# Optimization experiments

Hardware: AMD Instinct MI355X
Metric: run time of the kernel (lower is better)

The kernel has to match this reference:

```python
import jax, jax.numpy as jnp
import numpy as np

NUM_CLASSES = 96
T = 27          # max label slots per sample (hardcoded `range(1, 27)` in source)
NEG = -1e9      # finite stand-in for -inf masking (sim values are in [-1, 1])


def setup_inputs() -> dict:
    key = jax.random.key(0)
    k1, k2, k3 = jax.random.split(key, 3)
    B, D = 256, 1024
    input_f = jax.random.normal(k1, (B, T, D), dtype=jnp.float32)
    # labels in [1, 95]; zero is the end-of-word terminator
    tgt = jax.random.randint(k2, (B, T), 1, NUM_CLASSES, dtype=jnp.int32)
    lens = jax.random.randint(k3, (B,), 5, T, dtype=jnp.int32)  # first zero at position lens >= 1
    tgt = jnp.where(jnp.arange(T)[None, :] >= lens[:, None], 0, tgt)
    return {"input_f": input_f, "target": tgt}


def reference(input_f, target):
    B, Tt, D = input_f.shape
    # first zero position in target[:, 1:] gives the ragged prefix length per sample
    fz = jnp.argmax(target[:, 1:] == 0, axis=1) + 1            # [B], in [1, T-1]
    valid = jnp.arange(Tt)[None, :] < fz[:, None]              # [B, T] prefix mask (t=0 always valid)
    m = valid.reshape(-1)                                      # [B*T]

    # L2-normalize all rows (padded rows are masked out of the loss below)
    f = input_f.reshape(-1, D)
    f = f / jnp.clip(jnp.linalg.norm(f, axis=1, keepdims=True), 1e-12)
    sim = f @ f.T                                              # [N, N], N = B*T

    lab = target.reshape(-1)
    same = lab[:, None] == lab[None, :]                        # label_encode @ label_encode.T == 1
    pair_valid = m[:, None] & m[None, :]

    eye = jnp.eye(m.shape[0], dtype=bool)
    # multi-positive cross entropy (QDTrack-style):
    # loss_i = log(1 + sum_{pos p, neg n} exp(sim_in - sim_ip))
    #        = softplus(logsumexp_n(sim_in) + logsumexp_p(-sim_ip))
    pos_mask = (pair_valid & same) | (~m[:, None] & eye)       # give invalid rows a dummy entry
    neg_mask = (pair_valid & ~same) | (~m[:, None] & eye)
    lse_pos = jax.nn.logsumexp(jnp.where(pos_mask, -sim, NEG), axis=1)
    lse_neg = jax.nn.logsumexp(jnp.where(neg_mask, sim, NEG), axis=1)
    row_loss = jax.nn.softplus(lse_pos + lse_neg)

    n_valid = jnp.sum(m.astype(sim.dtype))
    return jnp.sum(jnp.where(m, row_loss, 0.0)) / n_valid
```

## Files before the change

kernel.cpp:

```cpp
#include <hip/hip_runtime.h>
#include <hip/hip_bf16.h>
#include <stdint.h>

#define BATCH 256
#define TSLOT 27
#define NTOT  (BATCH * TSLOT)
#define DIM   1024
#define TS    192
#define NSMAX 36
#define NTRIMAX (NSMAX * (NSMAX + 1) / 2)
#define KST   16
#define BUFSZ 24576
#define NBUF  6

typedef __attribute__((ext_vector_type(4))) float f32x4;
typedef __attribute__((ext_vector_type(2))) long l64x2;

__global__ __launch_bounds__(256) void prep_norm_kernel(const float* __restrict__ in,
                                                        const int* __restrict__ tgt,
                                                        unsigned char* __restrict__ cfb,
                                                        int* __restrict__ clab,
                                                        int* __restrict__ meta,
                                                        float* __restrict__ accum,
                                                        int* __restrict__ counter) {
    __shared__ int shs[256];
    __shared__ int shf[256];
    const int b = threadIdx.x;
    {
        const int* t = tgt + b * TSLOT;
        int fz = TSLOT;
        #pragma unroll
        for (int i = TSLOT - 1; i >= 1; --i) fz = (t[i] == 0) ? i : fz;
        shf[b] = fz;
        shs[b] = fz;
    }
    __syncthreads();
    for (int d = 1; d < 256; d <<= 1) {
        int v = (b >= d) ? shs[b - d] : 0;
        __syncthreads();
        shs[b] += v;
        __syncthreads();
    }
    const int nv = shs[255];
    const int npad = ((nv + TS - 1) / TS) * TS;

    if (blockIdx.x == 0) {
        if (b < 2) accum[b] = 0.0f;
        if (b == 2) *counter = 0;
        if (b == 3) { meta[0] = nv; meta[1] = npad; }
        if (b < npad - nv) clab[nv + b] = -1;
    }

    const int wv   = blockIdx.x * 4 + (threadIdx.x >> 6);
    const int lane = threadIdx.x & 63;
    const int bb = wv / TSLOT, tt = wv - bb * TSLOT;
    const int fzb = shf[bb];
    if (tt >= fzb) return;
    const int dest = (shs[bb] - fzb) + tt;

    const float* src = in + (size_t)wv * DIM + lane * 16;
    float4 v0 = *(const float4*)(src);
    float4 v1 = *(const float4*)(src + 4);
    float4 v2 = *(const float4*)(src + 8);
    float4 v3 = *(const float4*)(src + 12);
    float ss = v0.x*v0.x + v0.y*v0.y + v0.z*v0.z + v0.w*v0.w
             + v1.x*v1.x + v1.y*v1.y + v1.z*v1.z + v1.w*v1.w
             + v2.x*v2.x + v2.y*v2.y + v2.z*v2.z + v2.w*v2.w
             + v3.x*v3.x + v3.y*v3.y + v3.z*v3.z + v3.w*v3.w;
    #pragma unroll
    for (int off = 1; off < 64; off <<= 1) ss += __shfl_xor(ss, off);
    const float sc = 1.0f / fmaxf(sqrtf(ss), 1e-12f);
    float f[16] = {v0.x,v0.y,v0.z,v0.w, v1.x,v1.y,v1.z,v1.w,
                   v2.x,v2.y,v2.z,v2.w, v3.x,v3.y,v3.z,v3.w};
    uint4 o;
    unsigned int* ow = (unsigned int*)&o;
    #pragma unroll
    for (int q = 0; q < 4; ++q) {
        unsigned int u = 0;
        u = __builtin_amdgcn_cvt_pk_fp8_f32(f[q*4+0] * sc, f[q*4+1] * sc, u, 0);
        u = __builtin_amdgcn_cvt_pk_fp8_f32(f[q*4+2] * sc, f[q*4+3] * sc, u, 1);
        ow[q] = u;
    }
    *(uint4*)(cfb + (size_t)dest * DIM + lane * 16) = o;
    if (lane == 0) clab[dest] = tgt[wv];
}

__global__ __launch_bounds__(512) void gemm_kernel(const unsigned char* __restrict__ fb,
                                                   const int* __restrict__ clab,
                                                   const int* __restrict__ meta,
                                                   float* __restrict__ Ppos,
                                                   float* __restrict__ Pneg) {
    __shared__ __align__(16) char lds[NBUF * BUFSZ];

    const int npad = meta[1];
    const int nstrips = npad / TS;
    const int nact = nstrips * (nstrips + 1) / 2;
    const int k = blockIdx.x >> 3, x = blockIdx.x & 7;
    const int q8 = nact >> 3, r8 = nact & 7;
    const int cnt = q8 + (x < r8 ? 1 : 0);
    if (k >= cnt) return;
    int t = x * q8 + (x < r8 ? x : r8) + k;
    int bi = 0;
    while (t >= nstrips - bi) { t -= nstrips - bi; ++bi; }
    const int bj = bi + t;
    const int row0 = bi * TS;
    const int col0 = bj * TS;
    const bool diag = (bi == bj);

    const int tid  = threadIdx.x;
    const int lane = tid & 63;
    const int w    = tid >> 6;
    const int wm   = w >> 2;
    const int wn   = w & 3;

    f32x4 acc[6][3] = {};
    const char* fbyte = (const char*)fb;

    auto stage = [&](int s) {
        char* buf = lds + (s % NBUF) * BUFSZ;
        const int k0b = s * 64;
        #pragma unroll
        for (int j = 0; j < 3; ++j) {
            const int c = w * 192 + j * 64 + lane;
            const int cc = (c >= 768) ? c - 768 : c;
            const int base = (c >= 768) ? col0 : row0;
            const int r = cc >> 2, ks = cc & 3;
            const char* g = fbyte + (size_t)(base + r) * DIM + k0b + ks * 16;
            __builtin_amdgcn_global_load_lds(
                (const __attribute__((address_space(1))) void*)g,
                (__attribute__((address_space(3))) void*)(buf + c * 16),
                16, 0, 0);
        }
    };

    const int rsel = lane & 15, tsl = lane >> 4;
    auto compute = [&](int s) {
        const char* bA = lds + (s % NBUF) * BUFSZ;
        const char* bB = bA + 12288;
        l64x2 av[6], bv[3];
        #pragma unroll
        for (int m = 0; m < 6; ++m) {
            const int r = wm * 96 + m * 16 + rsel;
            av[m] = *(const l64x2*)(bA + r * 64 + tsl * 16);
        }
        #pragma unroll
        for (int n = 0; n < 3; ++n) {
            const int r = wn * 48 + n * 16 + rsel;
            bv[n] = *(const l64x2*)(bB + r * 64 + tsl * 16);
        }
        #pragma unroll
        for (int kk = 0; kk < 2; ++kk)
            #pragma unroll
            for (int m = 0; m < 6; ++m)
                #pragma unroll
                for (int n = 0; n < 3; ++n)
                    acc[m][n] = __builtin_amdgcn_mfma_f32_16x16x32_fp8_fp8(
                        av[m][kk], bv[n][kk], acc[m][n], 0, 0, 0);
    };

    stage(0); stage(1); stage(2); stage(3); stage(4);
    #pragma unroll 1
    for (int s = 0; s < KST - 5; ++s) {
        asm volatile("s_waitcnt vmcnt(12)" ::: "memory");
        __builtin_amdgcn_s_barrier();
        asm volatile("" ::: "memory");
        stage(s + 5);
        compute(s);
    }
    asm volatile("s_waitcnt vmcnt(12)" ::: "memory");
    __builtin_amdgcn_s_barrier();
    asm volatile("" ::: "memory");
    compute(KST - 5);
    asm volatile("s_waitcnt vmcnt(9)" ::: "memory");
    __builtin_amdgcn_s_barrier();
    asm volatile("" ::: "memory");
    compute(KST - 4);
    asm volatile("s_waitcnt vmcnt(6)" ::: "memory");
    __builtin_amdgcn_s_barrier();
    asm volatile("" ::: "memory");
    compute(KST - 3);
    asm volatile("s_waitcnt vmcnt(3)" ::: "memory");
    __builtin_amdgcn_s_barrier();
    asm volatile("" ::: "memory");
    compute(KST - 2);
    asm volatile("s_waitcnt vmcnt(0)" ::: "memory");
    __builtin_amdgcn_s_barrier();
    asm volatile("" ::: "memory");
    compute(KST - 1);

    const int c = rsel, g = tsl;
    float cpos[3] = {0, 0, 0}, cneg[3] = {0, 0, 0};
    float* fl = (float*)lds;

    #pragma unroll
    for (int m = 0; m < 6; ++m) {
        #pragma unroll
        for (int rg = 0; rg < 4; ++rg) {
            const int gi = row0 + wm * 96 + m * 16 + g * 4 + rg;
            const int li = clab[gi];
            float rp = 0.0f, rn = 0.0f;
            #pragma unroll
            for (int n = 0; n < 3; ++n) {
                const int gj = col0 + wn * 48 + n * 16 + c;
                const int lj = clab[gj];
                const float s = acc[m][n][rg];
                if (li >= 0 && lj >= 0) {
                    if (li == lj) { float e = __expf(-s); rp += e; cpos[n] += e; }
                    else          { float e = __expf(s);  rn += e; cneg[n] += e; }
                }
            }
            #pragma unroll
            for (int off = 1; off <= 8; off <<= 1) {
                rp += __shfl_xor(rp, off);
                rn += __shfl_xor(rn, off);
            }
            if (c == 0) {
                int lr = m * 16 + g * 4 + rg;
                fl[w * 96 + lr]        = rp;
                fl[768 + w * 96 + lr]  = rn;
            }
        }
    }
    #pragma unroll
    for (int n = 0; n < 3; ++n) {
        float p = cpos[n], q = cneg[n];
        p += __shfl_xor(p, 16); p += __shfl_xor(p, 32);
        q += __shfl_xor(q, 16); q += __shfl_xor(q, 32);
        if (g == 0) {
            int lc = n * 16 + c;
            fl[1536 + w * 48 + lc] = p;
            fl[1920 + w * 48 + lc] = q;
        }
    }
    __syncthreads();
    if (tid < 192) {
        int sm = tid / 96, lr = tid % 96;
        float rp = 0.0f, rn = 0.0f;
        #pragma unroll
        for (int kk = 0; kk < 4; ++kk) {
            rp += fl[(sm * 4 + kk) * 96 + lr];
            rn += fl[768 + (sm * 4 + kk) * 96 + lr];
        }
        int gi = row0 + tid;
        Ppos[(size_t)bj * NTOT + gi] = rp;
        Pneg[(size_t)bj * NTOT + gi] = rn;
    } else if (tid < 384 && !diag) {
        int j = tid - 192, cn = j / 48, lc = j % 48;
        float p = fl[1536 + cn * 48 + lc] + fl[1536 + (4 + cn) * 48 + lc];
        float q = fl[1920 + cn * 48 + lc] + fl[1920 + (4 + cn) * 48 + lc];
        int gj = col0 + j;
        Ppos[(size_t)bi * NTOT + gj] = p;
        Pneg[(size_t)bi * NTOT + gj] = q;
    }
}

__global__ __launch_bounds__(256) void finalize_kernel(const int* __restrict__ clab,
                                                       const int* __restrict__ meta,
                                                       const float* __restrict__ Ppos,
                                                       const float* __restrict__ Pneg,
                                                       float* __restrict__ accum,
                                                       int* __restrict__ counter,
                                                       float* __restrict__ out) {
    int i = blockIdx.x * blockDim.x + threadIdx.x;
    const int npad = meta[1];
    const int nta = npad / TS;
    float s = 0.0f, cnt = 0.0f;
    if (i < npad && clab[i] >= 0) {
        float sp = 0.0f, sn = 0.0f;
        for (int t = 0; t < nta; ++t) {
            sp += Ppos[(size_t)t * NTOT + i];
            sn += Pneg[(size_t)t * NTOT + i];
        }
        s = log1pf(sp * sn);
        cnt = 1.0f;
    }
    #pragma unroll
    for (int off = 1; off < 64; off <<= 1) {
        s   += __shfl_xor(s, off);
        cnt += __shfl_xor(cnt, off);
    }
    __shared__ float sh[8];
    int lane = threadIdx.x & 63, w = threadIdx.x >> 6;
    if (lane == 0) { sh[w] = s; sh[4 + w] = cnt; }
    __syncthreads();
    if (threadIdx.x == 0) {
        atomicAdd(&accum[0], sh[0] + sh[1] + sh[2] + sh[3]);
        atomicAdd(&accum[1], sh[4] + sh[5] + sh[6] + sh[7]);
        __threadfence();
        int done = atomicAdd(counter, 1);
        if (done == (int)gridDim.x - 1) {
            __threadfence();
            out[0] = accum[0] / accum[1];
        }
    }
}

extern "C" void kernel_launch(void* const* d_in, const int* in_sizes, int n_in,
                              void* d_out, int out_size, void* d_ws, size_t ws_size,
                              hipStream_t stream) {
    (void)in_sizes; (void)n_in; (void)out_size; (void)ws_size;
    const float* input_f = (const float*)d_in[0];
    const int*   target  = (const int*)d_in[1];
    float* out = (float*)d_out;

    char* ws = (char*)d_ws;
    const size_t FB_BYTES = (size_t)NTOT * DIM;
    unsigned char* cfb = (unsigned char*)ws;
    char* p = ws + FB_BYTES;
    int*   clab  = (int*)p;            p += NTOT * 4;
    int*   meta  = (int*)p;            p += 256;
    float* accum = (float*)p;          p += 128;
    int*   counter = (int*)p;          p += 128;
    float* Ppos  = (float*)p;          p += (size_t)NSMAX * NTOT * 4;
    float* Pneg  = (float*)p;

    prep_norm_kernel<<<dim3(NTOT / 4), dim3(256), 0, stream>>>(input_f, target, cfb, clab, meta, accum, counter);
    gemm_kernel<<<dim3(NTRIMAX), dim3(512), 0, stream>>>(cfb, clab, meta, Ppos, Pneg);
    finalize_kernel<<<dim3((NTOT + 255) / 256), dim3(256), 0, stream>>>(clab, meta, Ppos, Pneg, accum, counter, out);
}
```

Measured before the change: 50.08 us.

## Fuse prep, GEMM and finalize into one cooperative persistent kernel

```diff
diff --git a/kernel.cpp b/kernel.cpp
--- a/kernel.cpp
+++ b/kernel.cpp
@@ -1,6 +1,9 @@
 #include <hip/hip_runtime.h>
 #include <hip/hip_bf16.h>
+#include <hip/hip_cooperative_groups.h>
 #include <stdint.h>
+
+namespace cg = cooperative_groups;
 
 #define BATCH 256
 #define TSLOT 27
@@ -8,289 +11,290 @@
 #define DIM   1024
 #define TS    192
 #define NSMAX 36
-#define NTRIMAX (NSMAX * (NSMAX + 1) / 2)
 #define KST   16
 #define BUFSZ 24576
 #define NBUF  6
+#define NBLK  256
 
 typedef __attribute__((ext_vector_type(4))) float f32x4;
 typedef __attribute__((ext_vector_type(2))) long l64x2;
 
-__global__ __launch_bounds__(256) void prep_norm_kernel(const float* __restrict__ in,
-                                                        const int* __restrict__ tgt,
-                                                        unsigned char* __restrict__ cfb,
-                                                        int* __restrict__ clab,
-                                                        int* __restrict__ meta,
-                                                        float* __restrict__ accum,
-                                                        int* __restrict__ counter) {
+__global__ __launch_bounds__(512, 1)
+void fused_kernel(const float* __restrict__ in,
+                  const int* __restrict__ tgt,
+                  unsigned char* __restrict__ cfb,
+                  int* __restrict__ clab,
+                  float* __restrict__ Ppos,
+                  float* __restrict__ Pneg,
+                  float* __restrict__ accum,
+                  int* __restrict__ counter,
+                  float* __restrict__ out) {
+    __shared__ __align__(16) char lds[NBUF * BUFSZ];
     __shared__ int shs[256];
     __shared__ int shf[256];
-    const int b = threadIdx.x;
-    {
-        const int* t = tgt + b * TSLOT;
+
+    const int tid  = threadIdx.x;
+    const int lane = tid & 63;
+    const int w    = tid >> 6;
+    cg::grid_group grid = cg::this_grid();
+
+    if (tid < 256) {
+        const int* t = tgt + tid * TSLOT;
         int fz = TSLOT;
         #pragma unroll
         for (int i = TSLOT - 1; i >= 1; --i) fz = (t[i] == 0) ? i : fz;
-        shf[b] = fz;
-        shs[b] = fz;
+        shf[tid] = fz;
+        shs[tid] = fz;
     }
     __syncthreads();
     for (int d = 1; d < 256; d <<= 1) {
-        int v = (b >= d) ? shs[b - d] : 0;
+        int v = 0;
+        if (tid < 256 && tid >= d) v = shs[tid - d];
         __syncthreads();
-        shs[b] += v;
+        if (tid < 256) shs[tid] += v;
         __syncthreads();
     }
     const int nv = shs[255];
     const int npad = ((nv + TS - 1) / TS) * TS;
+    const int nstrips = npad / TS;
 
     if (blockIdx.x == 0) {
-        if (b < 2) accum[b] = 0.0f;
-        if (b == 2) *counter = 0;
-        if (b == 3) { meta[0] = nv; meta[1] = npad; }
-        if (b < npad - nv) clab[nv + b] = -1;
-    }
-
-    const int wv   = blockIdx.x * 4 + (threadIdx.x >> 6);
-    const int lane = threadIdx.x & 63;
-    const int bb = wv / TSLOT, tt = wv - bb * TSLOT;
-    const int fzb = shf[bb];
-    if (tt >= fzb) return;
-    const int dest = (shs[bb] - fzb) + tt;
-
-    const float* src = in + (size_t)wv * DIM + lane * 16;
-    float4 v0 = *(const float4*)(src);
-    float4 v1 = *(const float4*)(src + 4);
-    float4 v2 = *(const float4*)(src + 8);
-    float4 v3 = *(const float4*)(src + 12);
-    float ss = v0.x*v0.x + v0.y*v0.y + v0.z*v0.z + v0.w*v0.w
-             + v1.x*v1.x + v1.y*v1.y + v1.z*v1.z + v1.w*v1.w
-             + v2.x*v2.x + v2.y*v2.y + v2.z*v2.z + v2.w*v2.w
-             + v3.x*v3.x + v3.y*v3.y + v3.z*v3.z + v3.w*v3.w;
-    #pragma unroll
-    for (int off = 1; off < 64; off <<= 1) ss += __shfl_xor(ss, off);
-    const float sc = 1.0f / fmaxf(sqrtf(ss), 1e-12f);
-    float f[16] = {v0.x,v0.y,v0.z,v0.w, v1.x,v1.y,v1.z,v1.w,
-                   v2.x,v2.y,v2.z,v2.w, v3.x,v3.y,v3.z,v3.w};
-    uint4 o;
-    unsigned int* ow = (unsigned int*)&o;
-    #pragma unroll
-    for (int q = 0; q < 4; ++q) {
-        unsigned int u = 0;
-        u = __builtin_amdgcn_cvt_pk_fp8_f32(f[q*4+0] * sc, f[q*4+1] * sc, u, 0);
-        u = __builtin_amdgcn_cvt_pk_fp8_f32(f[q*4+2] * sc, f[q*4+3] * sc, u, 1);
-        ow[q] = u;
-    }
-    *(uint4*)(cfb + (size_t)dest * DIM + lane * 16) = o;
-    if (lane == 0) clab[dest] = tgt[wv];
-}
-
-__global__ __launch_bounds__(512) void gemm_kernel(const unsigned char* __restrict__ fb,
-                                                   const int* __restrict__ clab,
-                                                   const int* __restrict__ meta,
-                                                   float* __restrict__ Ppos,
-                                                   float* __restrict__ Pneg) {
-    __shared__ __align__(16) char lds[NBUF * BUFSZ];
-
-    const int npad = meta[1];
-    const int nstrips = npad / TS;
-    const int nact = nstrips * (nstrips + 1) / 2;
-    const int k = blockIdx.x >> 3, x = blockIdx.x & 7;
-    const int q8 = nact >> 3, r8 = nact & 7;
-    const int cnt = q8 + (x < r8 ? 1 : 0);
-    if (k >= cnt) return;
-    int t = x * q8 + (x < r8 ? x : r8) + k;
-    int bi = 0;
-    while (t >= nstrips - bi) { t -= nstrips - bi; ++bi; }
-    const int bj = bi + t;
-    const int row0 = bi * TS;
-    const int col0 = bj * TS;
-    const bool diag = (bi == bj);
-
-    const int tid  = threadIdx.x;
-    const int lane = tid & 63;
-    const int w    = tid >> 6;
-    const int wm   = w >> 2;
-    const int wn   = w & 3;
-
-    f32x4 acc[6][3] = {};
-    const char* fbyte = (const char*)fb;
-
-    auto stage = [&](int s) {
-        char* buf = lds + (s % NBUF) * BUFSZ;
-        const int k0b = s * 64;
+        if (tid < 2) accum[tid] = 0.0f;
+        if (tid == 2) *counter = 0;
+        if (tid < npad - nv) clab[nv + tid] = -1;
+    }
+
+    for (int wv = blockIdx.x * 8 + w; wv < NTOT; wv += NBLK * 8) {
+        const int bb = wv / TSLOT, tt = wv - bb * TSLOT;
+        const int fzb = shf[bb];
+        if (tt >= fzb) continue;
+        const int dest = (shs[bb] - fzb) + tt;
+
+        const float* src = in + (size_t)wv * DIM + lane * 16;
+        float4 v0 = *(const float4*)(src);
+        float4 v1 = *(const float4*)(src + 4);
+        float4 v2 = *(const float4*)(src + 8);
+        float4 v3 = *(const float4*)(src + 12);
+        float ss = v0.x*v0.x + v0.y*v0.y + v0.z*v0.z + v0.w*v0.w
+                 + v1.x*v1.x + v1.y*v1.y + v1.z*v1.z + v1.w*v1.w
+                 + v2.x*v2.x + v2.y*v2.y + v2.z*v2.z + v2.w*v2.w
+                 + v3.x*v3.x + v3.y*v3.y + v3.z*v3.z + v3.w*v3.w;
         #pragma unroll
-        for (int j = 0; j < 3; ++j) {
-            const int c = w * 192 + j * 64 + lane;
-            const int cc = (c >= 768) ? c - 768 : c;
-            const int base = (c >= 768) ? col0 : row0;
-            const int r = cc >> 2, ks = cc & 3;
-            const char* g = fbyte + (size_t)(base + r) * DIM + k0b + ks * 16;
-            __builtin_amdgcn_global_load_lds(
-                (const __attribute__((address_space(1))) void*)g,
-                (__attribute__((address_space(3))) void*)(buf + c * 16),
-                16, 0, 0);
-        }
-    };
-
-    const int rsel = lane & 15, tsl = lane >> 4;
-    auto compute = [&](int s) {
-        const char* bA = lds + (s % NBUF) * BUFSZ;
-        const char* bB = bA + 12288;
-        l64x2 av[6], bv[3];
+        for (int off = 1; off < 64; off <<= 1) ss += __shfl_xor(ss, off);
+        const float sc = 1.0f / fmaxf(sqrtf(ss), 1e-12f);
+        float f[16] = {v0.x,v0.y,v0.z,v0.w, v1.x,v1.y,v1.z,v1.w,
+                       v2.x,v2.y,v2.z,v2.w, v3.x,v3.y,v3.z,v3.w};
+        uint4 o;
+        unsigned int* ow = (unsigned int*)&o;
         #pragma unroll
-        for (int m = 0; m < 6; ++m) {
-            const int r = wm * 96 + m * 16 + rsel;
-            av[m] = *(const l64x2*)(bA + r * 64 + tsl * 16);
-        }
-        #pragma unroll
-        for (int n = 0; n < 3; ++n) {
-            const int r = wn * 48 + n * 16 + rsel;
-            bv[n] = *(const l64x2*)(bB + r * 64 + tsl * 16);
-        }
-        #pragma unroll
-        for (int kk = 0; kk < 2; ++kk)
+        for (int q = 0; q < 4; ++q) {
+            unsigned int u = 0;
+            u = __builtin_amdgcn_cvt_pk_fp8_f32(f[q*4+0] * sc, f[q*4+1] * sc, u, 0);
+            u = __builtin_amdgcn_cvt_pk_fp8_f32(f[q*4+2] * sc, f[q*4+3] * sc, u, 1);
+            ow[q] = u;
+        }
+        *(uint4*)(cfb + (size_t)dest * DIM + lane * 16) = o;
+        if (lane == 0) clab[dest] = tgt[wv];
+    }
+
+    grid.sync();
+
+    {
+        const int nact = nstrips * (nstrips + 1) / 2;
+        const int x = blockIdx.x & 7, kb0 = blockIdx.x >> 3;
+        const int q8 = nact >> 3, r8 = nact & 7;
+        const int cnt = q8 + (x < r8 ? 1 : 0);
+        const int wm = w >> 2;
+        const int wn = w & 3;
+        const int rsel = lane & 15, tsl = lane >> 4;
+        const char* fbyte = (const char*)cfb;
+
+        for (int kt = kb0; kt < cnt; kt += 32) {
+            int t = x * q8 + (x < r8 ? x : r8) + kt;
+            int bi = 0;
+            while (t >= nstrips - bi) { t -= nstrips - bi; ++bi; }
+            const int bj = bi + t;
+            const int row0 = bi * TS;
+            const int col0 = bj * TS;
+            const bool diag = (bi == bj);
+
+            f32x4 acc[6][3] = {};
+
+            auto stage = [&](int s) {
+                char* buf = lds + (s % NBUF) * BUFSZ;
+                const int k0b = s * 64;
+                #pragma unroll
+                for (int j = 0; j < 3; ++j) {
+                    const int c = w * 192 + j * 64 + lane;
+                    const int cc = (c >= 768) ? c - 768 : c;
+                    const int base = (c >= 768) ? col0 : row0;
+                    const int r = cc >> 2, ks = cc & 3;
+                    const char* g = fbyte + (size_t)(base + r) * DIM + k0b + ks * 16;
+                    __builtin_amdgcn_global_load_lds(
+                        (const __attribute__((address_space(1))) void*)g,
+                        (__attribute__((address_space(3))) void*)(buf + c * 16),
+                        16, 0, 0);
+                }
+            };
+            auto compute = [&](int s) {
+                const char* bA = lds + (s % NBUF) * BUFSZ;
+                const char* bB = bA + 12288;
+                l64x2 av[6], bv[3];
+                #pragma unroll
+                for (int m = 0; m < 6; ++m) {
+                    const int r = wm * 96 + m * 16 + rsel;
+                    av[m] = *(const l64x2*)(bA + r * 64 + tsl * 16);
+                }
+                #pragma unroll
+                for (int n = 0; n < 3; ++n) {
+                    const int r = wn * 48 + n * 16 + rsel;
+                    bv[n] = *(const l64x2*)(bB + r * 64 + tsl * 16);
+                }
+                #pragma unroll
+                for (int kk = 0; kk < 2; ++kk)
+                    #pragma unroll
+                    for (int m = 0; m < 6; ++m)
+                        #pragma unroll
+                        for (int n = 0; n < 3; ++n)
+                            acc[m][n] = __builtin_amdgcn_mfma_f32_16x16x32_fp8_fp8(
+                                av[m][kk], bv[n][kk], acc[m][n], 0, 0, 0);
+            };
+
+            stage(0); stage(1); stage(2); stage(3); stage(4);
+            #pragma unroll 1
+            for (int s = 0; s < KST - 5; ++s) {
+                asm volatile("s_waitcnt vmcnt(12)" ::: "memory");
+                __builtin_amdgcn_s_barrier();
+                asm volatile("" ::: "memory");
+                stage(s + 5);
+                compute(s);
+            }
+            asm volatile("s_waitcnt vmcnt(12)" ::: "memory");
+            __builtin_amdgcn_s_barrier();
+            asm volatile("" ::: "memory");
+            compute(KST - 5);
+            asm volatile("s_waitcnt vmcnt(9)" ::: "memory");
+            __builtin_amdgcn_s_barrier();
+            asm volatile("" ::: "memory");
+            compute(KST - 4);
+            asm volatile("s_waitcnt vmcnt(6)" ::: "memory");
+            __builtin_amdgcn_s_barrier();
+            asm volatile("" ::: "memory");
+            compute(KST - 3);
+            asm volatile("s_waitcnt vmcnt(3)" ::: "memory");
+            __builtin_amdgcn_s_barrier();
+            asm volatile("" ::: "memory");
+            compute(KST - 2);
+            asm volatile("s_waitcnt vmcnt(0)" ::: "memory");
+            __builtin_amdgcn_s_barrier();
+            asm volatile("" ::: "memory");
+            compute(KST - 1);
+
+            const int c = rsel, g = tsl;
+            float cpos[3] = {0, 0, 0}, cneg[3] = {0, 0, 0};
+            float* fl = (float*)lds;
+
             #pragma unroll
-            for (int m = 0; m < 6; ++m)
-                #pragma unroll
-                for (int n = 0; n < 3; ++n)
-                    acc[m][n] = __builtin_amdgcn_mfma_f32_16x16x32_fp8_fp8(
-                        av[m][kk], bv[n][kk], acc[m][n], 0, 0, 0);
-    };
-
-    stage(0); stage(1); stage(2); stage(3); stage(4);
-    #pragma unroll 1
-    for (int s = 0; s < KST - 5; ++s) {
-        asm volatile("s_waitcnt vmcnt(12)" ::: "memory");
-        __builtin_amdgcn_s_barrier();
-        asm volatile("" ::: "memory");
-        stage(s + 5);
-        compute(s);
-    }
-    asm volatile("s_waitcnt vmcnt(12)" ::: "memory");
-    __builtin_amdgcn_s_barrier();
-    asm volatile("" ::: "memory");
-    compute(KST - 5);
-    asm volatile("s_waitcnt vmcnt(9)" ::: "memory");
-    __builtin_amdgcn_s_barrier();
-    asm volatile("" ::: "memory");
-    compute(KST - 4);
-    asm volatile("s_waitcnt vmcnt(6)" ::: "memory");
-    __builtin_amdgcn_s_barrier();
-    asm volatile("" ::: "memory");
-    compute(KST - 3);
-    asm volatile("s_waitcnt vmcnt(3)" ::: "memory");
-    __builtin_amdgcn_s_barrier();
-    asm volatile("" ::: "memory");
-    compute(KST - 2);
-    asm volatile("s_waitcnt vmcnt(0)" ::: "memory");
-    __builtin_amdgcn_s_barrier();
-    asm volatile("" ::: "memory");
-    compute(KST - 1);
-
-    const int c = rsel, g = tsl;
-    float cpos[3] = {0, 0, 0}, cneg[3] = {0, 0, 0};
-    float* fl = (float*)lds;
-
-    #pragma unroll
-    for (int m = 0; m < 6; ++m) {
-        #pragma unroll
-        for (int rg = 0; rg < 4; ++rg) {
-            const int gi = row0 + wm * 96 + m * 16 + g * 4 + rg;
-            const int li = clab[gi];
-            float rp = 0.0f, rn = 0.0f;
+            for (int m = 0; m < 6; ++m) {
+                #pragma unroll
+                for (int rg = 0; rg < 4; ++rg) {
+                    const int gi = row0 + wm * 96 + m * 16 + g * 4 + rg;
+                    const int li = clab[gi];
+                    float rp = 0.0f, rn = 0.0f;
+                    #pragma unroll
+                    for (int n = 0; n < 3; ++n) {
+                        const int gj = col0 + wn * 48 + n * 16 + c;
+                        const int lj = clab[gj];
+                        const float s = acc[m][n][rg];
+                        if (li >= 0 && lj >= 0) {
+                            if (li == lj) { float e = __expf(-s); rp += e; cpos[n] += e; }
+                            else          { float e = __expf(s);  rn += e; cneg[n] += e; }
+                        }
+                    }
+                    #pragma unroll
+                    for (int off = 1; off <= 8; off <<= 1) {
+                        rp += __shfl_xor(rp, off);
+                        rn += __shfl_xor(rn, off);
+                    }
+                    if (c == 0) {
+                        int lr = m * 16 + g * 4 + rg;
+                        fl[w * 96 + lr]        = rp;
+                        fl[768 + w * 96 + lr]  = rn;
+                    }
+                }
+            }
             #pragma unroll
             for (int n = 0; n < 3; ++n) {
-                const int gj = col0 + wn * 48 + n * 16 + c;
-                const int lj = clab[gj];
-                const float s = acc[m][n][rg];
-                if (li >= 0 && lj >= 0) {
-                    if (li == lj) { float e = __expf(-s); rp += e; cpos[n] += e; }
-                    else          { float e = __expf(s);  rn += e; cneg[n] += e; }
-                }
-            }
+                float p = cpos[n], q = cneg[n];
+                p += __shfl_xor(p, 16); p += __shfl_xor(p, 32);
+                q += __shfl_xor(q, 16); q += __shfl_xor(q, 32);
+                if (g == 0) {
+                    int lc = n * 16 + c;
+                    fl[1536 + w * 48 + lc] = p;
+                    fl[1920 + w * 48 + lc] = q;
+                }
+            }
+            __syncthreads();
+            if (tid < 192) {
+                int sm = tid / 96, lr = tid % 96;
+                float rp = 0.0f, rn = 0.0f;
+                #pragma unroll
+                for (int kk = 0; kk < 4; ++kk) {
+                    rp += fl[(sm * 4 + kk) * 96 + lr];
+                    rn += fl[768 + (sm * 4 + kk) * 96 + lr];
+                }
+                int gi = row0 + tid;
+                Ppos[(size_t)bj * NTOT + gi] = rp;
+                Pneg[(size_t)bj * NTOT + gi] = rn;
+            } else if (tid < 384 && !diag) {
+                int j = tid - 192, cn = j / 48, lc = j % 48;
+                float p = fl[1536 + cn * 48 + lc] + fl[1536 + (4 + cn) * 48 + lc];
+                float q = fl[1920 + cn * 48 + lc] + fl[1920 + (4 + cn) * 48 + lc];
+                int gj = col0 + j;
+                Ppos[(size_t)bi * NTOT + gj] = p;
+                Pneg[(size_t)bi * NTOT + gj] = q;
+            }
+            __syncthreads();
+        }
+    }
+
+    grid.sync();
+
+    {
+        const int nta = nstrips;
+        const int i = blockIdx.x * 512 + tid;
+        float s = 0.0f, cnt = 0.0f;
+        if (i < npad && clab[i] >= 0) {
+            float sp = 0.0f, sn = 0.0f;
+            for (int t = 0; t < nta; ++t) {
+                sp += Ppos[(size_t)t * NTOT + i];
+                sn += Pneg[(size_t)t * NTOT + i];
+            }
+            s = log1pf(sp * sn);
+            cnt = 1.0f;
+        }
+        #pragma unroll
+        for (int off = 1; off < 64; off <<= 1) {
+            s   += __shfl_xor(s, off);
+            cnt += __shfl_xor(cnt, off);
+        }
+        __shared__ float sh[16];
+        if (lane == 0) { sh[w] = s; sh[8 + w] = cnt; }
+        __syncthreads();
+        if (tid == 0) {
+            float ts = 0.0f, tc = 0.0f;
             #pragma unroll
-            for (int off = 1; off <= 8; off <<= 1) {
-                rp += __shfl_xor(rp, off);
-                rn += __shfl_xor(rn, off);
-            }
-            if (c == 0) {
-                int lr = m * 16 + g * 4 + rg;
-                fl[w * 96 + lr]        = rp;
-                fl[768 + w * 96 + lr]  = rn;
-            }
-        }
-    }
-    #pragma unroll
-    for (int n = 0; n < 3; ++n) {
-        float p = cpos[n], q = cneg[n];
-        p += __shfl_xor(p, 16); p += __shfl_xor(p, 32);
-        q += __shfl_xor(q, 16); q += __shfl_xor(q, 32);
-        if (g == 0) {
-            int lc = n * 16 + c;
-            fl[1536 + w * 48 + lc] = p;
-            fl[1920 + w * 48 + lc] = q;
-        }
-    }
-    __syncthreads();
-    if (tid < 192) {
-        int sm = tid / 96, lr = tid % 96;
-        float rp = 0.0f, rn = 0.0f;
-        #pragma unroll
-        for (int kk = 0; kk < 4; ++kk) {
-            rp += fl[(sm * 4 + kk) * 96 + lr];
-            rn += fl[768 + (sm * 4 + kk) * 96 + lr];
-        }
-        int gi = row0 + tid;
-        Ppos[(size_t)bj * NTOT + gi] = rp;
-        Pneg[(size_t)bj * NTOT + gi] = rn;
-    } else if (tid < 384 && !diag) {
-        int j = tid - 192, cn = j / 48, lc = j % 48;
-        float p = fl[1536 + cn * 48 + lc] + fl[1536 + (4 + cn) * 48 + lc];
-        float q = fl[1920 + cn * 48 + lc] + fl[1920 + (4 + cn) * 48 + lc];
-        int gj = col0 + j;
-        Ppos[(size_t)bi * NTOT + gj] = p;
-        Pneg[(size_t)bi * NTOT + gj] = q;
-    }
-}
-
-__global__ __launch_bounds__(256) void finalize_kernel(const int* __restrict__ clab,
-                                                       const int* __restrict__ meta,
-                                                       const float* __restrict__ Ppos,
-                                                       const float* __restrict__ Pneg,
-                                                       float* __restrict__ accum,
-                                                       int* __restrict__ counter,
-                                                       float* __restrict__ out) {
-    int i = blockIdx.x * blockDim.x + threadIdx.x;
-    const int npad = meta[1];
-    const int nta = npad / TS;
-    float s = 0.0f, cnt = 0.0f;
-    if (i < npad && clab[i] >= 0) {
-        float sp = 0.0f, sn = 0.0f;
-        for (int t = 0; t < nta; ++t) {
-            sp += Ppos[(size_t)t * NTOT + i];
-            sn += Pneg[(size_t)t * NTOT + i];
-        }
-        s = log1pf(sp * sn);
-        cnt = 1.0f;
-    }
-    #pragma unroll
-    for (int off = 1; off < 64; off <<= 1) {
-        s   += __shfl_xor(s, off);
-        cnt += __shfl_xor(cnt, off);
-    }
-    __shared__ float sh[8];
-    int lane = threadIdx.x & 63, w = threadIdx.x >> 6;
-    if (lane == 0) { sh[w] = s; sh[4 + w] = cnt; }
-    __syncthreads();
-    if (threadIdx.x == 0) {
-        atomicAdd(&accum[0], sh[0] + sh[1] + sh[2] + sh[3]);
-        atomicAdd(&accum[1], sh[4] + sh[5] + sh[6] + sh[7]);
-        __threadfence();
-        int done = atomicAdd(counter, 1);
-        if (done == (int)gridDim.x - 1) {
+            for (int k = 0; k < 8; ++k) { ts += sh[k]; tc += sh[8 + k]; }
+            if (tc > 0.0f || ts != 0.0f) {
+                atomicAdd(&accum[0], ts);
+                atomicAdd(&accum[1], tc);
+            }
             __threadfence();
-            out[0] = accum[0] / accum[1];
+            int done = atomicAdd(counter, 1);
+            if (done == NBLK - 1) {
+                __threadfence();
+                out[0] = accum[0] / accum[1];
+            }
         }
     }
 }
@@ -307,14 +311,15 @@
     const size_t FB_BYTES = (size_t)NTOT * DIM;
     unsigned char* cfb = (unsigned char*)ws;
     char* p = ws + FB_BYTES;
-    int*   clab  = (int*)p;            p += NTOT * 4;
-    int*   meta  = (int*)p;            p += 256;
-    float* accum = (float*)p;          p += 128;
+    int*   clab    = (int*)p;          p += NTOT * 4;
+    float* accum   = (float*)p;        p += 128;
     int*   counter = (int*)p;          p += 128;
-    float* Ppos  = (float*)p;          p += (size_t)NSMAX * NTOT * 4;
-    float* Pneg  = (float*)p;
-
-    prep_norm_kernel<<<dim3(NTOT / 4), dim3(256), 0, stream>>>(input_f, target, cfb, clab, meta, accum, counter);
-    gemm_kernel<<<dim3(NTRIMAX), dim3(512), 0, stream>>>(cfb, clab, meta, Ppos, Pneg);
-    finalize_kernel<<<dim3((NTOT + 255) / 256), dim3(256), 0, stream>>>(clab, meta, Ppos, Pneg, accum, counter, out);
+    float* Ppos    = (float*)p;        p += (size_t)NSMAX * NTOT * 4;
+    float* Pneg    = (float*)p;
+
+    void* kargs[] = {(void*)&input_f, (void*)&target, (void*)&cfb, (void*)&clab,
+                     (void*)&Ppos, (void*)&Pneg, (void*)&accum, (void*)&counter,
+                     (void*)&out};
+    hipLaunchCooperativeKernel((void*)fused_kernel, dim3(NBLK), dim3(512),
+                               kargs, 0, stream);
 }
```

Result: slower. 124.6 us (+148.9%).
